# Performance work log

Measured on AMD Instinct MI355X. Metric: run time of the kernel, lower is better.

Reference implementation:

```python
import jax, jax.numpy as jnp
import numpy as np

N, E, NMASK, NC = 50000, 600000, 10000, 16
DIMS = [128, 96, 64]
EPS = 1e-5


def _sage(x, src, dst, ew, deg_pos, Wp, bp, Ws, Wn, b):
    # DGL SAGEConv 'pool': m_e = relu(fc_pool(h_src)) * w_e ; neigh = max_e->v m_e
    p = jax.nn.relu(x @ Wp.T + bp)              # [N, din]
    m = p[src] * ew[:, None]                    # [E, din]
    neigh = jax.ops.segment_max(m, dst, num_segments=N)
    neigh = jnp.where(deg_pos, neigh, 0.0)      # zero in-degree -> 0 (DGL convention)
    return jax.nn.relu(x @ Ws.T + neigh @ Wn.T + b)


def setup_inputs() -> dict:
    key = jax.random.key(0)
    ks = iter(jax.random.split(key, 64))
    inp = {}
    inp["x"] = jax.random.normal(next(ks), (N, DIMS[0]), jnp.float32)
    inp["src"] = jax.random.randint(next(ks), (E,), 0, N)
    inp["dst"] = jax.random.randint(next(ks), (E,), 0, N)
    inp["ew"] = jax.random.uniform(next(ks), (E,), jnp.float32)
    inp["mask_nodes"] = jax.random.permutation(next(ks), N)[:NMASK]
    inp["mask_token"] = jax.random.normal(next(ks), (1, DIMS[0]), jnp.float32) * 0.02

    def lin(k, o, i):
        return jax.random.normal(k, (o, i), jnp.float32) * (1.0 / np.sqrt(i))

    enc_pairs = list(zip(DIMS[:-1], DIMS[1:]))              # (128,96),(96,64)
    dec_pairs = [(o, i) for (i, o) in reversed(enc_pairs)]  # (64,96),(96,128)
    for name, pairs in (("enc", enc_pairs), ("dec", dec_pairs)):
        for l, (di, do) in enumerate(pairs):
            inp[f"{name}{l}_Wp"] = lin(next(ks), di, di)
            inp[f"{name}{l}_bp"] = jnp.zeros((di,), jnp.float32)
            inp[f"{name}{l}_Ws"] = lin(next(ks), do, di)
            inp[f"{name}{l}_Wn"] = lin(next(ks), do, di)
            inp[f"{name}{l}_b"] = jnp.zeros((do,), jnp.float32)
    H = DIMS[-1]
    inp["W_e2d"] = lin(next(ks), H, H)
    inp["Wnp"] = lin(next(ks), NC, H)
    inp["bnp"] = jnp.zeros((NC,), jnp.float32)
    inp["ln_g"] = jnp.ones((NC,), jnp.float32)
    inp["ln_b"] = jnp.zeros((NC,), jnp.float32)
    return inp


def reference(x, src, dst, ew, mask_nodes, mask_token,
              enc0_Wp, enc0_bp, enc0_Ws, enc0_Wn, enc0_b,
              enc1_Wp, enc1_bp, enc1_Ws, enc1_Wn, enc1_b,
              dec0_Wp, dec0_bp, dec0_Ws, dec0_Wn, dec0_b,
              dec1_Wp, dec1_bp, dec1_Ws, dec1_Wn, dec1_b,
              W_e2d, Wnp, bnp, ln_g, ln_b):
    deg = jax.ops.segment_sum(jnp.ones((E,), jnp.float32), dst, num_segments=N)
    deg_pos = (deg > 0)[:, None]
    # mask: out_x[mask]=0 then += enc_mask_token  ==  set to token row
    h = x.at[mask_nodes].set(mask_token[0])
    h = _sage(h, src, dst, ew, deg_pos, enc0_Wp, enc0_bp, enc0_Ws, enc0_Wn, enc0_b)
    h = _sage(h, src, dst, ew, deg_pos, enc1_Wp, enc1_bp, enc1_Ws, enc1_Wn, enc1_b)
    # dropout(p=0) is identity
    z = h @ Wnp.T + bnp                              # node_pred linear
    mu = jnp.mean(z, -1, keepdims=True)
    var = jnp.var(z, -1, keepdims=True)
    n_scores = (z - mu) * jax.lax.rsqrt(var + EPS) * ln_g + ln_b
    r = h @ W_e2d.T                                  # encoder_to_decoder (no bias)
    r = _sage(r, src, dst, ew, deg_pos, dec0_Wp, dec0_bp, dec0_Ws, dec0_Wn, dec0_b)
    r = _sage(r, src, dst, ew, deg_pos, dec1_Wp, dec1_bp, dec1_Ws, dec1_Wn, dec1_b)
    return (r[mask_nodes], x[mask_nodes], n_scores)
```

## Files before the change

### kernel.cpp

```cpp
#include <hip/hip_runtime.h>

#define EPS_LN 1e-5f

typedef __attribute__((ext_vector_type(4))) float f32x4;
typedef __attribute__((ext_vector_type(4))) int i32x4;

__device__ inline unsigned short f2bf_rne(float x) {
  unsigned int u = __float_as_uint(x);
  unsigned int r = u + 0x7fffu + ((u >> 16) & 1u);
  return (unsigned short)(r >> 16);
}

__device__ inline float4 bf4_to_f4(uint2 u) {
  float4 f;
  f.x = __uint_as_float(u.x << 16);
  f.y = __uint_as_float(u.x & 0xffff0000u);
  f.z = __uint_as_float(u.y << 16);
  f.w = __uint_as_float(u.y & 0xffff0000u);
  return f;
}

__device__ inline uint2 f4_to_bf4(float4 v) {
  uint2 o;
  o.x = (unsigned)f2bf_rne(v.x) | ((unsigned)f2bf_rne(v.y) << 16);
  o.y = (unsigned)f2bf_rne(v.z) | ((unsigned)f2bf_rne(v.w) << 16);
  return o;
}

__device__ inline void split_bf16(float x, unsigned short& hi, unsigned short& lo) {
  unsigned int bits = __float_as_uint(x);
  hi = (unsigned short)(bits >> 16);
  float hif = __uint_as_float((unsigned int)hi << 16);
  float res = x - hif;
  lo = (unsigned short)(__float_as_uint(res) >> 16);
}

__device__ inline void mfma_b16(f32x4& acc, i32x4 a, i32x4 b) {
  asm volatile("v_mfma_f32_16x16x32_bf16 %0, %1, %2, %0"
               : "+v"(acc)
               : "v"(a), "v"(b));
}

struct SplitWArgs {
  const float* src[12];
  unsigned short* dh[12];
  unsigned short* dl[12];
  int n[12];
};

struct Prep1Args {
  const float4* x4; uint2* h_out; int n4; int cb_blocks;
  const int* dst; int* deg; int nE; int hist_blocks;
  const float* W10; const float* We2d; float* WpP;
  const float* W12; float* WsP;
};

__global__ __launch_bounds__(256) void prep1_kernel(Prep1Args a) {
  int b = blockIdx.x;
  int tid = threadIdx.x;
  if (b < a.cb_blocks) {
    int i = b * 256 + tid;
    if (i < a.n4) a.h_out[i] = f4_to_bf4(a.x4[i]);
    return;
  }
  b -= a.cb_blocks;
  if (b < a.hist_blocks) {
    int e = b * 256 + tid;
    if (e < a.nE) atomicAdd(a.deg + a.dst[e], 1);
    return;
  }
  b -= a.hist_blocks;
  if (b < 16) {
    int idx = b * 256 + tid;
    if (idx < 64 * 64) {
      int o = idx >> 6, i = idx & 63;
      float s = 0.f;
      for (int k = 0; k < 64; ++k) s += a.W10[o * 64 + k] * a.We2d[k * 64 + i];
      a.WpP[idx] = s;
    }
    return;
  }
  b -= 16;
  {
    int idx = b * 256 + tid;
    if (idx < 96 * 64) {
      int o = idx >> 6, i = idx & 63;
      float s = 0.f;
      for (int k = 0; k < 64; ++k) s += a.W12[o * 64 + k] * a.We2d[k * 64 + i];
      a.WsP[idx] = s;
    }
  }
}

#define SCAN_CHUNK 1024

struct Prep2Args {
  const int* deg; int* bsum; int n; int nb;
  const int* mn; const float* token; unsigned short* H; int nmask; int ms_blocks;
  SplitWArgs sw;
  int boff[13];
};

__global__ __launch_bounds__(256) void prep2_kernel(Prep2Args a) {
  __shared__ int red[256];
  int b = blockIdx.x;
  int tid = threadIdx.x;
  if (b < a.nb) {
    int base = b * SCAN_CHUNK;
    int s = 0;
#pragma unroll
    for (int t = 0; t < SCAN_CHUNK / 256; ++t) {
      int g = base + tid + t * 256;
      if (g < a.n) s += a.deg[g];
    }
    red[tid] = s;
    __syncthreads();
    for (int ofs = 128; ofs > 0; ofs >>= 1) {
      if (tid < ofs) red[tid] += red[tid + ofs];
      __syncthreads();
    }
    if (tid == 0) a.bsum[b] = red[0];
    return;
  }
  b -= a.nb;
  if (b < a.ms_blocks) {
    int gid = b * 256 + tid;
    if (gid >= a.nmask * 32) return;
    int i = gid >> 5;
    int c4 = (gid & 31) << 2;
    int r = a.mn[i];
    float4 t = *(const float4*)(a.token + c4);
    *(uint2*)(a.H + (size_t)r * 128 + c4) = f4_to_bf4(t);
    return;
  }
  b -= a.ms_blocks;
  {
    int m = 0;
    while (m < 11 && b >= a.boff[m + 1]) ++m;
    int i = ((b - a.boff[m]) * 256 + tid) * 4;
    if (i >= a.sw.n[m]) return;
    float4 v = *(const float4*)(a.sw.src[m] + i);
    unsigned short h[4], l[4];
    split_bf16(v.x, h[0], l[0]);
    split_bf16(v.y, h[1], l[1]);
    split_bf16(v.z, h[2], l[2]);
    split_bf16(v.w, h[3], l[3]);
    *(uint2*)(a.sw.dh[m] + i) = make_uint2((unsigned)h[0] | ((unsigned)h[1] << 16),
                                           (unsigned)h[2] | ((unsigned)h[3] << 16));
    *(uint2*)(a.sw.dl[m] + i) = make_uint2((unsigned)l[0] | ((unsigned)l[1] << 16),
                                           (unsigned)l[2] | ((unsigned)l[3] << 16));
  }
}

__global__ __launch_bounds__(64) void bscan_kernel(const int* __restrict__ bsum,
                                                   int* __restrict__ bbase,
                                                   int* __restrict__ off_n, int nb) {
  int tid = threadIdx.x;
  int v = (tid < nb) ? bsum[tid] : 0;
  int incl = v;
#pragma unroll
  for (int ofs = 1; ofs < 64; ofs <<= 1) {
    int u = __shfl_up(incl, ofs, 64);
    if (tid >= ofs) incl += u;
  }
  if (tid < nb) bbase[tid] = incl - v;
  if (tid == nb - 1) off_n[0] = incl;
}

__global__ __launch_bounds__(256) void chunkscan_kernel(const int* __restrict__ deg,
                                                        const int* __restrict__ bbase,
                                                        int* __restrict__ off, int n) {
  __shared__ int part[256];
  int tid = threadIdx.x;
  int base = blockIdx.x * SCAN_CHUNK;
  int g0 = base + tid * 4;
  int loc[4];
  int s = 0;
#pragma unroll
  for (int j = 0; j < 4; ++j) {
    int g = g0 + j;
    int d = (g < n) ? deg[g] : 0;
    loc[j] = s;
    s += d;
  }
  part[tid] = s;
  __syncthreads();
  for (int ofs = 1; ofs < 256; ofs <<= 1) {
    int v = 0;
    if (tid >= ofs) v = part[tid - ofs];
    __syncthreads();
    if (tid >= ofs) part[tid] += v;
    __syncthreads();
  }
  int pre = (tid == 0) ? 0 : part[tid - 1];
  int b = bbase[blockIdx.x] + pre;
#pragma unroll
  for (int j = 0; j < 4; ++j) {
    int g = g0 + j;
    if (g < n) off[g] = b + loc[j];
  }
}

__global__ __launch_bounds__(256) void scatter_kernel(const int* __restrict__ src,
                                                      const int* __restrict__ dst,
                                                      const float* __restrict__ ew,
                                                      const int* __restrict__ off,
                                                      int* __restrict__ cur,
                                                      int2* __restrict__ esw, int nE) {
  int e = blockIdx.x * 256 + threadIdx.x;
  if (e >= nE) return;
  int d = dst[e];
  int pos = off[d] + atomicAdd(cur + d, 1);
  esw[pos] = make_int2(src[e], __float_as_int(ew[e]));
}

__global__ __launch_bounds__(256) void neigh_csr_kernel(
    const unsigned short* __restrict__ P, const int* __restrict__ off,
    const int2* __restrict__ esw,
    unsigned short* __restrict__ neigh, int din, int lanes, int nN) {
  int gid = blockIdx.x * 256 + threadIdx.x;
  int v = gid / lanes;
  int c = (gid - v * lanes) << 3;
  if (v >= nN) return;
  int jlo = off[v], jhi = off[v + 1];
  float m[8];
#pragma unroll
  for (int t = 0; t < 8; ++t) m[t] = 0.f;
  float n1[8], n2[8], n3[8];
#pragma unroll
  for (int t = 0; t < 8; ++t) { n1[t] = 0.f; n2[t] = 0.f; n3[t] = 0.f; }
  int j = jlo;
  for (; j + 4 <= jhi; j += 4) {
    int2 e0 = esw[j], e1 = esw[j + 1], e2 = esw[j + 2], e3 = esw[j + 3];
    uint4 q0 = *(const uint4*)(P + (size_t)e0.x * din + c);
    uint4 q1 = *(const uint4*)(P + (size_t)e1.x * din + c);
    uint4 q2 = *(const uint4*)(P + (size_t)e2.x * din + c);
    uint4 q3 = *(const uint4*)(P + (size_t)e3.x * din + c);
    float w0 = __int_as_float(e0.y), w1 = __int_as_float(e1.y);
    float w2 = __int_as_float(e2.y), w3 = __int_as_float(e3.y);
    float4 a0 = bf4_to_f4(make_uint2(q0.x, q0.y)), b0 = bf4_to_f4(make_uint2(q0.z, q0.w));
    float4 a1 = bf4_to_f4(make_uint2(q1.x, q1.y)), b1 = bf4_to_f4(make_uint2(q1.z, q1.w));
    float4 a2 = bf4_to_f4(make_uint2(q2.x, q2.y)), b2 = bf4_to_f4(make_uint2(q2.z, q2.w));
    float4 a3 = bf4_to_f4(make_uint2(q3.x, q3.y)), b3 = bf4_to_f4(make_uint2(q3.z, q3.w));
    m[0] = fmaxf(m[0], a0.x * w0); m[1] = fmaxf(m[1], a0.y * w0);
    m[2] = fmaxf(m[2], a0.z * w0); m[3] = fmaxf(m[3], a0.w * w0);
    m[4] = fmaxf(m[4], b0.x * w0); m[5] = fmaxf(m[5], b0.y * w0);
    m[6] = fmaxf(m[6], b0.z * w0); m[7] = fmaxf(m[7], b0.w * w0);
    n1[0] = fmaxf(n1[0], a1.x * w1); n1[1] = fmaxf(n1[1], a1.y * w1);
    n1[2] = fmaxf(n1[2], a1.z * w1); n1[3] = fmaxf(n1[3], a1.w * w1);
    n1[4] = fmaxf(n1[4], b1.x * w1); n1[5] = fmaxf(n1[5], b1.y * w1);
    n1[6] = fmaxf(n1[6], b1.z * w1); n1[7] = fmaxf(n1[7], b1.w * w1);
    n2[0] = fmaxf(n2[0], a2.x * w2); n2[1] = fmaxf(n2[1], a2.y * w2);
    n2[2] = fmaxf(n2[2], a2.z * w2); n2[3] = fmaxf(n2[3], a2.w * w2);
    n2[4] = fmaxf(n2[4], b2.x * w2); n2[5] = fmaxf(n2[5], b2.y * w2);
    n2[6] = fmaxf(n2[6], b2.z * w2); n2[7] = fmaxf(n2[7], b2.w * w2);
    n3[0] = fmaxf(n3[0], a3.x * w3); n3[1] = fmaxf(n3[1], a3.y * w3);
    n3[2] = fmaxf(n3[2], a3.z * w3); n3[3] = fmaxf(n3[3], a3.w * w3);
    n3[4] = fmaxf(n3[4], b3.x * w3); n3[5] = fmaxf(n3[5], b3.y * w3);
    n3[6] = fmaxf(n3[6], b3.z * w3); n3[7] = fmaxf(n3[7], b3.w * w3);
  }
  for (; j < jhi; ++j) {
    int2 e = esw[j];
    float w = __int_as_float(e.y);
    uint4 q = *(const uint4*)(P + (size_t)e.x * din + c);
    float4 a = bf4_to_f4(make_uint2(q.x, q.y)), b = bf4_to_f4(make_uint2(q.z, q.w));
    m[0] = fmaxf(m[0], a.x * w); m[1] = fmaxf(m[1], a.y * w);
    m[2] = fmaxf(m[2], a.z * w); m[3] = fmaxf(m[3], a.w * w);
    m[4] = fmaxf(m[4], b.x * w); m[5] = fmaxf(m[5], b.y * w);
    m[6] = fmaxf(m[6], b.z * w); m[7] = fmaxf(m[7], b.w * w);
  }
#pragma unroll
  for (int t = 0; t < 8; ++t) m[t] = fmaxf(fmaxf(m[t], n1[t]), fmaxf(n2[t], n3[t]));
  uint2 o0 = f4_to_bf4(make_float4(m[0], m[1], m[2], m[3]));
  uint2 o1 = f4_to_bf4(make_float4(m[4], m[5], m[6], m[7]));
  *(uint4*)(neigh + (size_t)v * din + c) = make_uint4(o0.x, o0.y, o1.x, o1.y);
}

template <int TNT>
__global__ __launch_bounds__(256) void mfma_gemm_kernel(
    const unsigned short* __restrict__ A1, const unsigned short* __restrict__ Wh1,
    const unsigned short* __restrict__ Wl1, int k1,
    const float* __restrict__ bias,
    unsigned short* __restrict__ C, int nrows) {
  constexpr int BN = TNT * 16;
  constexpr int WS = 136;
  __shared__ __align__(16) unsigned short Wh[BN][WS];
  __shared__ __align__(16) unsigned short Wl[BN][WS];

  const int tid = threadIdx.x;
  const int lane = tid & 63;
  const int wv = tid >> 6;
  const int lr = lane & 15;
  const int lg = lane >> 4;
  const int row0 = blockIdx.x * 64;
  const int gra = row0 + wv * 16 + lr;

  f32x4 acc[TNT];
#pragma unroll
  for (int t = 0; t < TNT; ++t) acc[t] = (f32x4)(0.f);

  {
    int tot8 = BN * k1 / 8;
    for (int i = tid; i < tot8; i += 256) {
      int e0 = i * 8;
      int col = e0 / k1;
      int kk = e0 - col * k1;
      *(uint4*)&Wh[col][kk] = *(const uint4*)(Wh1 + e0);
      *(uint4*)&Wl[col][kk] = *(const uint4*)(Wl1 + e0);
    }
  }
  __syncthreads();

  for (int cb = 0; cb < k1; cb += 32) {
    i32x4 a_h = (i32x4)(0);
    if (gra < nrows) a_h = *(const i32x4*)(A1 + (size_t)gra * k1 + cb + lg * 8);
#pragma unroll
    for (int t = 0; t < TNT; ++t) {
      i32x4 b_h = *(const i32x4*)&Wh[t * 16 + lr][cb + lg * 8];
      i32x4 b_l = *(const i32x4*)&Wl[t * 16 + lr][cb + lg * 8];
      mfma_b16(acc[t], a_h, b_h);
      mfma_b16(acc[t], a_h, b_l);
    }
  }

  asm volatile("s_nop 7\n\ts_nop 7" ::);

#pragma unroll
  for (int t = 0; t < TNT; ++t) {
    int c = t * 16 + lr;
    float bv = bias[c];
#pragma unroll
    for (int q = 0; q < 4; ++q) {
      int r = row0 + wv * 16 + lg * 4 + q;
      if (r < nrows) {
        float v = fmaxf(acc[t][q] + bv, 0.f);
        C[(size_t)r * BN + c] = f2bf_rne(v);
      }
    }
  }
}

template <int TNT>
__global__ __launch_bounds__(256) void mfma_gemm_fused_kernel(
    const unsigned short* __restrict__ A1, const unsigned short* __restrict__ Wh1,
    const unsigned short* __restrict__ Wl1,
    const unsigned short* __restrict__ A2, const unsigned short* __restrict__ Wh2,
    const unsigned short* __restrict__ Wl2, int K,
    const float* __restrict__ bias, unsigned short* __restrict__ C,
    const unsigned short* __restrict__ pWh, const unsigned short* __restrict__ pWl,
    const float* __restrict__ pBias, unsigned short* __restrict__ P_out,
    int nrows) {
  constexpr int BN = TNT * 16;
  constexpr int WS = 136;
  __shared__ __align__(16) unsigned short Wh[BN][WS];
  __shared__ __align__(16) unsigned short Wl[BN][WS];

  const int tid = threadIdx.x;
  const int lane = tid & 63;
  const int wv = tid >> 6;
  const int lr = lane & 15;
  const int lg = lane >> 4;
  const int row0 = blockIdx.x * 64;
  const int gra = row0 + wv * 16 + lr;

  f32x4 acc[TNT];
#pragma unroll
  for (int t = 0; t < TNT; ++t) acc[t] = (f32x4)(0.f);

  for (int pass = 0; pass < 2; ++pass) {
    const unsigned short* A = pass ? A2 : A1;
    const unsigned short* Whp = pass ? Wh2 : Wh1;
    const unsigned short* Wlp = pass ? Wl2 : Wl1;

    if (pass) __syncthreads();
    {
      int tot8 = BN * K / 8;
      for (int i = tid; i < tot8; i += 256) {
        int e0 = i * 8;
        int col = e0 / K;
        int kk = e0 - col * K;
        *(uint4*)&Wh[col][kk] = *(const uint4*)(Whp + e0);
        *(uint4*)&Wl[col][kk] = *(const uint4*)(Wlp + e0);
      }
    }
    __syncthreads();

    for (int cb = 0; cb < K; cb += 32) {
      i32x4 a_h = (i32x4)(0);
      if (gra < nrows) a_h = *(const i32x4*)(A + (size_t)gra * K + cb + lg * 8);
#pragma unroll
      for (int t = 0; t < TNT; ++t) {
        i32x4 b_h = *(const i32x4*)&Wh[t * 16 + lr][cb + lg * 8];
        i32x4 b_l = *(const i32x4*)&Wl[t * 16 + lr][cb + lg * 8];
        mfma_b16(acc[t], a_h, b_h);
        mfma_b16(acc[t], a_h, b_l);
      }
    }
  }

  asm volatile("s_nop 7\n\ts_nop 7" ::);

#pragma unroll
  for (int t = 0; t < TNT; ++t) {
    int c = t * 16 + lr;
    float bv = bias[c];
#pragma unroll
    for (int q = 0; q < 4; ++q) {
      int r = row0 + wv * 16 + lg * 4 + q;
      if (r < nrows) {
        float v = fmaxf(acc[t][q] + bv, 0.f);
        C[(size_t)r * BN + c] = f2bf_rne(v);
      }
    }
  }

  if (P_out == nullptr) return;

  __syncthreads();
  {
    int tot8 = BN * BN / 8;
    for (int i = tid; i < tot8; i += 256) {
      int e0 = i * 8;
      int col = e0 / BN;
      int kk = e0 - col * BN;
      *(uint4*)&Wh[col][kk] = *(const uint4*)(pWh + e0);
      *(uint4*)&Wl[col][kk] = *(const uint4*)(pWl + e0);
    }
  }
  __syncthreads();

#pragma unroll
  for (int t = 0; t < TNT; ++t) acc[t] = (f32x4)(0.f);

  for (int cb = 0; cb < BN; cb += 32) {
    i32x4 a_h = (i32x4)(0);
    if (gra < nrows) a_h = *(const i32x4*)(C + (size_t)gra * BN + cb + lg * 8);
#pragma unroll
    for (int t = 0; t < TNT; ++t) {
      i32x4 b_h = *(const i32x4*)&Wh[t * 16 + lr][cb + lg * 8];
      i32x4 b_l = *(const i32x4*)&Wl[t * 16 + lr][cb + lg * 8];
      mfma_b16(acc[t], a_h, b_h);
      mfma_b16(acc[t], a_h, b_l);
    }
  }

  asm volatile("s_nop 7\n\ts_nop 7" ::);

#pragma unroll
  for (int t = 0; t < TNT; ++t) {
    int c = t * 16 + lr;
    float bv = pBias[c];
#pragma unroll
    for (int q = 0; q < 4; ++q) {
      int r = row0 + wv * 16 + lg * 4 + q;
      if (r < nrows) {
        float v = fmaxf(acc[t][q] + bv, 0.f);
        P_out[(size_t)r * BN + c] = f2bf_rne(v);
      }
    }
  }
}

__global__ __launch_bounds__(256) void nodepred_ln_kernel(
    const unsigned short* __restrict__ H, const float* __restrict__ Wnp,
    const float* __restrict__ bnp, const float* __restrict__ g,
    const float* __restrict__ lb, float* __restrict__ out, int nrows) {
  __shared__ float hs[16][64];
  int tid = threadIdx.x;
  int row0 = blockIdx.x * 16;
  {
    int r = tid >> 4;
    int c4 = (tid & 15) << 2;
    int gr = row0 + r;
    float4 v = make_float4(0.f, 0.f, 0.f, 0.f);
    if (gr < nrows) v = bf4_to_f4(*(const uint2*)(H + (size_t)gr * 64 + c4));
    *(float4*)&hs[r][c4] = v;
  }
  __syncthreads();
  int r = tid >> 4, j = tid & 15;
  float z = bnp[j];
  const float* wrow = Wnp + j * 64;
#pragma unroll 8
  for (int k = 0; k < 64; ++k) z += hs[r][k] * wrow[k];
  float s = z, s2 = z * z;
#pragma unroll
  for (int m = 1; m < 16; m <<= 1) {
    s += __shfl_xor(s, m, 16);
    s2 += __shfl_xor(s2, m, 16);
  }
  float mu = s * (1.f / 16.f);
  float var = s2 * (1.f / 16.f) - mu * mu;
  float o = (z - mu) * rsqrtf(var + EPS_LN) * g[j] + lb[j];
  int gr = row0 + r;
  if (gr < nrows) out[(size_t)gr * 16 + j] = o;
}

__global__ __launch_bounds__(256) void gather_out_kernel(
    const int* __restrict__ mn, const unsigned short* __restrict__ R,
    const float* __restrict__ X,
    float* __restrict__ o1, float* __restrict__ o2, int nmask) {
  int gid = blockIdx.x * 256 + threadIdx.x;
  if (gid >= nmask * 32) return;
  int i = gid >> 5, c4 = (gid & 31) << 2;
  int r = mn[i];
  float4 rv = bf4_to_f4(*(const uint2*)(R + (size_t)r * 128 + c4));
  *(float4*)(o1 + (size_t)i * 128 + c4) = rv;
  *(float4*)(o2 + (size_t)i * 128 + c4) = *(const float4*)(X + (size_t)r * 128 + c4);
}

static void launch_fused(const unsigned short* A1, const unsigned short* Wh1,
                         const unsigned short* Wl1,
                         const unsigned short* A2, const unsigned short* Wh2,
                         const unsigned short* Wl2, int K,
                         const float* bias, unsigned short* C,
                         const unsigned short* pWh, const unsigned short* pWl,
                         const float* pBias, unsigned short* P_out,
                         int m, int nrows, hipStream_t s) {
  int blocks = (nrows + 63) / 64;
  switch (m) {
    case 128:
      mfma_gemm_fused_kernel<8><<<blocks, 256, 0, s>>>(A1, Wh1, Wl1, A2, Wh2, Wl2, K,
                                                       bias, C, pWh, pWl, pBias, P_out, nrows);
      break;
    case 96:
      mfma_gemm_fused_kernel<6><<<blocks, 256, 0, s>>>(A1, Wh1, Wl1, A2, Wh2, Wl2, K,
                                                       bias, C, pWh, pWl, pBias, P_out, nrows);
      break;
    case 64:
      mfma_gemm_fused_kernel<4><<<blocks, 256, 0, s>>>(A1, Wh1, Wl1, A2, Wh2, Wl2, K,
                                                       bias, C, pWh, pWl, pBias, P_out, nrows);
      break;
  }
}

extern "C" void kernel_launch(void* const* d_in, const int* in_sizes, int n_in,
                              void* d_out, int out_size, void* d_ws, size_t ws_size,
                              hipStream_t stream) {
  const float* x = (const float*)d_in[0];
  const int* src = (const int*)d_in[1];
  const int* dst = (const int*)d_in[2];
  const float* ew = (const float*)d_in[3];
  const int* mn = (const int*)d_in[4];
  const float* token = (const float*)d_in[5];

  const float* W[20];
  for (int i = 0; i < 20; ++i) W[i] = (const float*)d_in[6 + i];
  const float* W_e2d = (const float*)d_in[26];
  const float* Wnp = (const float*)d_in[27];
  const float* bnp = (const float*)d_in[28];
  const float* ln_g = (const float*)d_in[29];
  const float* ln_b = (const float*)d_in[30];

  const int Nn = in_sizes[0] / 128;
  const int E = in_sizes[1];
  const int nmask = in_sizes[4];
  const int nb = (Nn + SCAN_CHUNK - 1) / SCAN_CHUNK;

  unsigned short* bufA = (unsigned short*)d_ws;
  unsigned short* bufB = bufA + (size_t)Nn * 128;
  unsigned short* pool16 = bufB + (size_t)Nn * 128;
  unsigned short* neigh16 = pool16 + (size_t)Nn * 128;
  int* deg = (int*)(neigh16 + (size_t)Nn * 128);
  int* cur = deg + Nn;
  int2* esw = (int2*)(cur + Nn);
  int* off = (int*)(esw + E);
  int* bsum = off + Nn + 1;
  int* bbase = bsum + 64;
  float* WpP = (float*)(bbase + 64);
  float* WsP = WpP + 64 * 64;
  unsigned short* wplanes =
      (unsigned short*)(((uintptr_t)(WsP + 96 * 64) + 15) & ~(uintptr_t)15);

  const int msz[12] = {128 * 128, 96 * 128, 96 * 128, 96 * 96, 64 * 96, 64 * 96,
                       64 * 64,  96 * 64,  96 * 64,  96 * 96, 128 * 96, 128 * 96};
  const float* msrc[12] = {W[0], W[2], W[3], W[5], W[7], W[8],
                           WpP,  WsP,  W[13], W[15], W[17], W[18]};
  int mtot = 0;
  int moff[12];
  for (int i = 0; i < 12; ++i) { moff[i] = mtot; mtot += msz[i]; }
  unsigned short* wh_[12];
  unsigned short* wl_[12];
  for (int i = 0; i < 12; ++i) {
    wh_[i] = wplanes + moff[i];
    wl_[i] = wplanes + mtot + moff[i];
  }

  hipMemsetAsync(deg, 0, (size_t)Nn * 2 * sizeof(int), stream);

  Prep1Args p1;
  p1.x4 = (const float4*)x;
  p1.h_out = (uint2*)bufA;
  p1.n4 = Nn * 128 / 4;
  p1.cb_blocks = (p1.n4 + 255) / 256;
  p1.dst = dst;
  p1.deg = deg;
  p1.nE = E;
  p1.hist_blocks = (E + 255) / 256;
  p1.W10 = W[10]; p1.We2d = W_e2d; p1.WpP = WpP;
  p1.W12 = W[12]; p1.WsP = WsP;
  int p1_blocks = p1.cb_blocks + p1.hist_blocks + 16 + 24;
  prep1_kernel<<<p1_blocks, 256, 0, stream>>>(p1);

  Prep2Args p2;
  p2.deg = deg; p2.bsum = bsum; p2.n = Nn; p2.nb = nb;
  p2.mn = mn; p2.token = token; p2.H = bufA; p2.nmask = nmask;
  p2.ms_blocks = (nmask * 32 + 255) / 256;
  for (int i = 0; i < 12; ++i) {
    p2.sw.src[i] = msrc[i];
    p2.sw.dh[i] = wh_[i];
    p2.sw.dl[i] = wl_[i];
    p2.sw.n[i] = msz[i];
  }
  p2.boff[0] = 0;
  for (int i = 0; i < 12; ++i) p2.boff[i + 1] = p2.boff[i] + (msz[i] / 4 + 255) / 256;
  int p2_blocks = p2.nb + p2.ms_blocks + p2.boff[12];
  prep2_kernel<<<p2_blocks, 256, 0, stream>>>(p2);

  bscan_kernel<<<1, 64, 0, stream>>>(bsum, bbase, off + Nn, nb);
  chunkscan_kernel<<<nb, 256, 0, stream>>>(deg, bbase, off, Nn);
  scatter_kernel<<<(E + 255) / 256, 256, 0, stream>>>(src, dst, ew, off, cur, esw, E);

  int gblocks = (Nn + 63) / 64;

  mfma_gemm_kernel<8><<<gblocks, 256, 0, stream>>>(bufA, wh_[0], wl_[0], 128, W[1],
                                                   pool16, Nn);

  auto neigh = [&](int din) {
    int lanes = din >> 3;
    long long tot = (long long)Nn * lanes;
    int nblocks = (int)((tot + 255) / 256);
    neigh_csr_kernel<<<nblocks, 256, 0, stream>>>(pool16, off, esw, neigh16, din, lanes, Nn);
  };

  neigh(128);
  launch_fused(bufA, wh_[1], wl_[1], neigh16, wh_[2], wl_[2], 128, W[4], bufB,
               wh_[3], wl_[3], W[6], pool16, 96, Nn, stream);

  neigh(96);
  launch_fused(bufB, wh_[4], wl_[4], neigh16, wh_[5], wl_[5], 96, W[9], bufA,
               wh_[6], wl_[6], W[11], pool16, 64, Nn, stream);

  float* out_r = (float*)d_out;
  float* out_x = out_r + (size_t)nmask * 128;
  float* out_ns = out_x + (size_t)nmask * 128;
  nodepred_ln_kernel<<<(Nn + 15) / 16, 256, 0, stream>>>(bufA, Wnp, bnp, ln_g, ln_b, out_ns, Nn);

  neigh(64);
  launch_fused(bufA, wh_[7], wl_[7], neigh16, wh_[8], wl_[8], 64, W[14], bufB,
               wh_[9], wl_[9], W[16], pool16, 96, Nn, stream);

  neigh(96);
  launch_fused(bufB, wh_[10], wl_[10], neigh16, wh_[11], wl_[11], 96, W[19], bufA,
               nullptr, nullptr, nullptr, nullptr, 128, Nn, stream);

  gather_out_kernel<<<(nmask * 32 + 255) / 256, 256, 0, stream>>>(mn, bufA, x, out_r, out_x, nmask);
}
```

Before: 337.7 us.

## Merge independent kernels into combined launches to cut launch count

Folds the single-block bscan into chunkscan, so each block redoes the 64-entry block-sum scan itself. The edge scatter and the first pool GEMM become one launch split by block index, and so do the layer-2 neighbor max (din=64) and the node-pred LayerNorm. The intent is to remove kernel launches and inter-kernel gaps, and to let independent work overlap on the GPU. The cost is a larger LDS footprint for the scatter blocks in the combined kernel, which may lower occupancy, plus redundant tiny scans per block.

```diff
diff --git a/kernel.cpp b/kernel.cpp
--- a/kernel.cpp
+++ b/kernel.cpp
@@ -152,26 +152,24 @@
   }
 }
 
-__global__ __launch_bounds__(64) void bscan_kernel(const int* __restrict__ bsum,
-                                                   int* __restrict__ bbase,
-                                                   int* __restrict__ off_n, int nb) {
+__global__ __launch_bounds__(256) void chunkscan_kernel(const int* __restrict__ deg,
+                                                        const int* __restrict__ bsum,
+                                                        int* __restrict__ off,
+                                                        int n, int nb) {
+  __shared__ int part[256];
+  __shared__ int basesh;
   int tid = threadIdx.x;
-  int v = (tid < nb) ? bsum[tid] : 0;
-  int incl = v;
-#pragma unroll
-  for (int ofs = 1; ofs < 64; ofs <<= 1) {
-    int u = __shfl_up(incl, ofs, 64);
-    if (tid >= ofs) incl += u;
-  }
-  if (tid < nb) bbase[tid] = incl - v;
-  if (tid == nb - 1) off_n[0] = incl;
-}
-
-__global__ __launch_bounds__(256) void chunkscan_kernel(const int* __restrict__ deg,
-                                                        const int* __restrict__ bbase,
-                                                        int* __restrict__ off, int n) {
-  __shared__ int part[256];
-  int tid = threadIdx.x;
+  if (tid < 64) {
+    int v = (tid < nb) ? bsum[tid] : 0;
+    int incl = v;
+#pragma unroll
+    for (int ofs = 1; ofs < 64; ofs <<= 1) {
+      int u = __shfl_up(incl, ofs, 64);
+      if (tid >= ofs) incl += u;
+    }
+    if (tid == (int)blockIdx.x) basesh = incl - v;
+    if (blockIdx.x == 0 && tid == nb - 1) off[n] = incl;
+  }
   int base = blockIdx.x * SCAN_CHUNK;
   int g0 = base + tid * 4;
   int loc[4];
@@ -193,7 +191,7 @@
     __syncthreads();
   }
   int pre = (tid == 0) ? 0 : part[tid - 1];
-  int b = bbase[blockIdx.x] + pre;
+  int b = basesh + pre;
 #pragma unroll
   for (int j = 0; j < 4; ++j) {
     int g = g0 + j;
@@ -201,24 +199,83 @@
   }
 }
 
-__global__ __launch_bounds__(256) void scatter_kernel(const int* __restrict__ src,
-                                                      const int* __restrict__ dst,
-                                                      const float* __restrict__ ew,
-                                                      const int* __restrict__ off,
-                                                      int* __restrict__ cur,
-                                                      int2* __restrict__ esw, int nE) {
-  int e = blockIdx.x * 256 + threadIdx.x;
-  if (e >= nE) return;
-  int d = dst[e];
-  int pos = off[d] + atomicAdd(cur + d, 1);
-  esw[pos] = make_int2(src[e], __float_as_int(ew[e]));
-}
-
-__global__ __launch_bounds__(256) void neigh_csr_kernel(
-    const unsigned short* __restrict__ P, const int* __restrict__ off,
-    const int2* __restrict__ esw,
-    unsigned short* __restrict__ neigh, int din, int lanes, int nN) {
-  int gid = blockIdx.x * 256 + threadIdx.x;
+struct ComboAArgs {
+  const int* src; const int* dst; const float* ew;
+  const int* off; int* cur; int2* esw; int nE; int sc_blocks;
+  const unsigned short* A1; const unsigned short* Wh1; const unsigned short* Wl1;
+  const float* bias; unsigned short* C; int nrows;
+};
+
+__global__ __launch_bounds__(256) void comboA_kernel(ComboAArgs a) {
+  __shared__ __align__(16) unsigned short Wh[128][136];
+  __shared__ __align__(16) unsigned short Wl[128][136];
+  int b = blockIdx.x;
+  int tid = threadIdx.x;
+  if (b < a.sc_blocks) {
+    int e = b * 256 + tid;
+    if (e >= a.nE) return;
+    int d = a.dst[e];
+    int pos = a.off[d] + atomicAdd(a.cur + d, 1);
+    a.esw[pos] = make_int2(a.src[e], __float_as_int(a.ew[e]));
+    return;
+  }
+  b -= a.sc_blocks;
+  constexpr int K = 128;
+  const int lane = tid & 63;
+  const int wv = tid >> 6;
+  const int lr = lane & 15;
+  const int lg = lane >> 4;
+  const int row0 = b * 64;
+  const int gra = row0 + wv * 16 + lr;
+
+  f32x4 acc[8];
+#pragma unroll
+  for (int t = 0; t < 8; ++t) acc[t] = (f32x4)(0.f);
+
+  {
+    int tot8 = 128 * K / 8;
+    for (int i = tid; i < tot8; i += 256) {
+      int e0 = i * 8;
+      int col = e0 / K;
+      int kk = e0 - col * K;
+      *(uint4*)&Wh[col][kk] = *(const uint4*)(a.Wh1 + e0);
+      *(uint4*)&Wl[col][kk] = *(const uint4*)(a.Wl1 + e0);
+    }
+  }
+  __syncthreads();
+
+  for (int cb = 0; cb < K; cb += 32) {
+    i32x4 a_h = (i32x4)(0);
+    if (gra < a.nrows) a_h = *(const i32x4*)(a.A1 + (size_t)gra * K + cb + lg * 8);
+#pragma unroll
+    for (int t = 0; t < 8; ++t) {
+      i32x4 b_h = *(const i32x4*)&Wh[t * 16 + lr][cb + lg * 8];
+      i32x4 b_l = *(const i32x4*)&Wl[t * 16 + lr][cb + lg * 8];
+      mfma_b16(acc[t], a_h, b_h);
+      mfma_b16(acc[t], a_h, b_l);
+    }
+  }
+
+  asm volatile("s_nop 7\n\ts_nop 7" ::);
+
+#pragma unroll
+  for (int t = 0; t < 8; ++t) {
+    int c = t * 16 + lr;
+    float bv = a.bias[c];
+#pragma unroll
+    for (int q = 0; q < 4; ++q) {
+      int r = row0 + wv * 16 + lg * 4 + q;
+      if (r < a.nrows) {
+        float v = fmaxf(acc[t][q] + bv, 0.f);
+        a.C[(size_t)r * 128 + c] = f2bf_rne(v);
+      }
+    }
+  }
+}
+
+__device__ inline void neigh_body(int gid, const unsigned short* P, const int* off,
+                                  const int2* esw, unsigned short* neigh,
+                                  int din, int lanes, int nN) {
   int v = gid / lanes;
   int c = (gid - v * lanes) << 3;
   if (v >= nN) return;
@@ -276,68 +333,56 @@
   *(uint4*)(neigh + (size_t)v * din + c) = make_uint4(o0.x, o0.y, o1.x, o1.y);
 }
 
-template <int TNT>
-__global__ __launch_bounds__(256) void mfma_gemm_kernel(
-    const unsigned short* __restrict__ A1, const unsigned short* __restrict__ Wh1,
-    const unsigned short* __restrict__ Wl1, int k1,
-    const float* __restrict__ bias,
-    unsigned short* __restrict__ C, int nrows) {
-  constexpr int BN = TNT * 16;
-  constexpr int WS = 136;
-  __shared__ __align__(16) unsigned short Wh[BN][WS];
-  __shared__ __align__(16) unsigned short Wl[BN][WS];
-
-  const int tid = threadIdx.x;
-  const int lane = tid & 63;
-  const int wv = tid >> 6;
-  const int lr = lane & 15;
-  const int lg = lane >> 4;
-  const int row0 = blockIdx.x * 64;
-  const int gra = row0 + wv * 16 + lr;
-
-  f32x4 acc[TNT];
-#pragma unroll
-  for (int t = 0; t < TNT; ++t) acc[t] = (f32x4)(0.f);
-
+__global__ __launch_bounds__(256) void neigh_csr_kernel(
+    const unsigned short* __restrict__ P, const int* __restrict__ off,
+    const int2* __restrict__ esw,
+    unsigned short* __restrict__ neigh, int din, int lanes, int nN) {
+  int gid = blockIdx.x * 256 + threadIdx.x;
+  neigh_body(gid, P, off, esw, neigh, din, lanes, nN);
+}
+
+struct ComboBArgs {
+  const unsigned short* P; const int* off; const int2* esw;
+  unsigned short* neigh; int nN; int ng_blocks;
+  const unsigned short* H; const float* Wnp; const float* bnp;
+  const float* g; const float* lb; float* out;
+};
+
+__global__ __launch_bounds__(256) void comboB_kernel(ComboBArgs a) {
+  __shared__ float hs[16][64];
+  int b = blockIdx.x;
+  int tid = threadIdx.x;
+  if (b < a.ng_blocks) {
+    neigh_body(b * 256 + tid, a.P, a.off, a.esw, a.neigh, 64, 8, a.nN);
+    return;
+  }
+  b -= a.ng_blocks;
+  int row0 = b * 16;
   {
-    int tot8 = BN * k1 / 8;
-    for (int i = tid; i < tot8; i += 256) {
-      int e0 = i * 8;
-      int col = e0 / k1;
-      int kk = e0 - col * k1;
-      *(uint4*)&Wh[col][kk] = *(const uint4*)(Wh1 + e0);
-      *(uint4*)&Wl[col][kk] = *(const uint4*)(Wl1 + e0);
-    }
+    int r = tid >> 4;
+    int c4 = (tid & 15) << 2;
+    int gr = row0 + r;
+    float4 v = make_float4(0.f, 0.f, 0.f, 0.f);
+    if (gr < a.nN) v = bf4_to_f4(*(const uint2*)(a.H + (size_t)gr * 64 + c4));
+    *(float4*)&hs[r][c4] = v;
   }
   __syncthreads();
-
-  for (int cb = 0; cb < k1; cb += 32) {
-    i32x4 a_h = (i32x4)(0);
-    if (gra < nrows) a_h = *(const i32x4*)(A1 + (size_t)gra * k1 + cb + lg * 8);
-#pragma unroll
-    for (int t = 0; t < TNT; ++t) {
-      i32x4 b_h = *(const i32x4*)&Wh[t * 16 + lr][cb + lg * 8];
-      i32x4 b_l = *(const i32x4*)&Wl[t * 16 + lr][cb + lg * 8];
-      mfma_b16(acc[t], a_h, b_h);
-      mfma_b16(acc[t], a_h, b_l);
-    }
-  }
-
-  asm volatile("s_nop 7\n\ts_nop 7" ::);
-
-#pragma unroll
-  for (int t = 0; t < TNT; ++t) {
-    int c = t * 16 + lr;
-    float bv = bias[c];
-#pragma unroll
-    for (int q = 0; q < 4; ++q) {
-      int r = row0 + wv * 16 + lg * 4 + q;
-      if (r < nrows) {
-        float v = fmaxf(acc[t][q] + bv, 0.f);
-        C[(size_t)r * BN + c] = f2bf_rne(v);
-      }
-    }
-  }
+  int r = tid >> 4, j = tid & 15;
+  float z = a.bnp[j];
+  const float* wrow = a.Wnp + j * 64;
+#pragma unroll 8
+  for (int k = 0; k < 64; ++k) z += hs[r][k] * wrow[k];
+  float s = z, s2 = z * z;
+#pragma unroll
+  for (int m = 1; m < 16; m <<= 1) {
+    s += __shfl_xor(s, m, 16);
+    s2 += __shfl_xor(s2, m, 16);
+  }
+  float mu = s * (1.f / 16.f);
+  float var = s2 * (1.f / 16.f) - mu * mu;
+  float o = (z - mu) * rsqrtf(var + EPS_LN) * a.g[j] + a.lb[j];
+  int gr = row0 + r;
+  if (gr < a.nN) a.out[(size_t)gr * 16 + j] = o;
 }
 
 template <int TNT>
@@ -459,40 +504,6 @@
       }
     }
   }
-}
-
-__global__ __launch_bounds__(256) void nodepred_ln_kernel(
-    const unsigned short* __restrict__ H, const float* __restrict__ Wnp,
-    const float* __restrict__ bnp, const float* __restrict__ g,
-    const float* __restrict__ lb, float* __restrict__ out, int nrows) {
-  __shared__ float hs[16][64];
-  int tid = threadIdx.x;
-  int row0 = blockIdx.x * 16;
-  {
-    int r = tid >> 4;
-    int c4 = (tid & 15) << 2;
-    int gr = row0 + r;
-    float4 v = make_float4(0.f, 0.f, 0.f, 0.f);
-    if (gr < nrows) v = bf4_to_f4(*(const uint2*)(H + (size_t)gr * 64 + c4));
-    *(float4*)&hs[r][c4] = v;
-  }
-  __syncthreads();
-  int r = tid >> 4, j = tid & 15;
-  float z = bnp[j];
-  const float* wrow = Wnp + j * 64;
-#pragma unroll 8
-  for (int k = 0; k < 64; ++k) z += hs[r][k] * wrow[k];
-  float s = z, s2 = z * z;
-#pragma unroll
-  for (int m = 1; m < 16; m <<= 1) {
-    s += __shfl_xor(s, m, 16);
-    s2 += __shfl_xor(s2, m, 16);
-  }
-  float mu = s * (1.f / 16.f);
-  float var = s2 * (1.f / 16.f) - mu * mu;
-  float o = (z - mu) * rsqrtf(var + EPS_LN) * g[j] + lb[j];
-  int gr = row0 + r;
-  if (gr < nrows) out[(size_t)gr * 16 + j] = o;
 }
 
 __global__ __launch_bounds__(256) void gather_out_kernel(
@@ -565,8 +576,7 @@
   int2* esw = (int2*)(cur + Nn);
   int* off = (int*)(esw + E);
   int* bsum = off + Nn + 1;
-  int* bbase = bsum + 64;
-  float* WpP = (float*)(bbase + 64);
+  float* WpP = (float*)(bsum + 64);
   float* WsP = WpP + 64 * 64;
   unsigned short* wplanes =
       (unsigned short*)(((uintptr_t)(WsP + 96 * 64) + 15) & ~(uintptr_t)15);
@@ -616,14 +626,16 @@
   int p2_blocks = p2.nb + p2.ms_blocks + p2.boff[12];
   prep2_kernel<<<p2_blocks, 256, 0, stream>>>(p2);
 
-  bscan_kernel<<<1, 64, 0, stream>>>(bsum, bbase, off + Nn, nb);
-  chunkscan_kernel<<<nb, 256, 0, stream>>>(deg, bbase, off, Nn);
-  scatter_kernel<<<(E + 255) / 256, 256, 0, stream>>>(src, dst, ew, off, cur, esw, E);
-
+  chunkscan_kernel<<<nb, 256, 0, stream>>>(deg, bsum, off, Nn, nb);
+
+  ComboAArgs ca;
+  ca.src = src; ca.dst = dst; ca.ew = ew;
+  ca.off = off; ca.cur = cur; ca.esw = esw; ca.nE = E;
+  ca.sc_blocks = (E + 255) / 256;
+  ca.A1 = bufA; ca.Wh1 = wh_[0]; ca.Wl1 = wl_[0];
+  ca.bias = W[1]; ca.C = pool16; ca.nrows = Nn;
   int gblocks = (Nn + 63) / 64;
-
-  mfma_gemm_kernel<8><<<gblocks, 256, 0, stream>>>(bufA, wh_[0], wl_[0], 128, W[1],
-                                                   pool16, Nn);
+  comboA_kernel<<<ca.sc_blocks + gblocks, 256, 0, stream>>>(ca);
 
   auto neigh = [&](int din) {
     int lanes = din >> 3;
@@ -643,9 +655,14 @@
   float* out_r = (float*)d_out;
   float* out_x = out_r + (size_t)nmask * 128;
   float* out_ns = out_x + (size_t)nmask * 128;
-  nodepred_ln_kernel<<<(Nn + 15) / 16, 256, 0, stream>>>(bufA, Wnp, bnp, ln_g, ln_b, out_ns, Nn);
-
-  neigh(64);
+
+  ComboBArgs cb;
+  cb.P = pool16; cb.off = off; cb.esw = esw; cb.neigh = neigh16; cb.nN = Nn;
+  cb.ng_blocks = (Nn * 8 + 255) / 256;
+  cb.H = bufA; cb.Wnp = Wnp; cb.bnp = bnp; cb.g = ln_g; cb.lb = ln_b; cb.out = out_ns;
+  int np_blocks = (Nn + 15) / 16;
+  comboB_kernel<<<cb.ng_blocks + np_blocks, 256, 0, stream>>>(cb);
+
   launch_fused(bufA, wh_[7], wl_[7], neigh16, wh_[8], wl_[8], 64, W[14], bufB,
                wh_[9], wl_[9], W[16], pool16, 96, Nn, stream);
 
```

Result: faster. 320.7 us (-5.0%).
